# Performance work log

Measured on AMD Instinct MI355X. Metric: run time of the kernel, lower is better.

The kernel has to match this reference:

```python
import jax, jax.numpy as jnp
import numpy as np

B, LQ, LKV = 4, 512, 8192
Q_DIM, KV_DIM = 1024, 512
QK_CH, V_CH, N_HEADS = 256, 256, 8
EPS = 1e-5


def _layernorm(x, g, b):
    m = jnp.mean(x, axis=-1, keepdims=True)
    v = jnp.mean(jnp.square(x - m), axis=-1, keepdims=True)
    return (x - m) * jax.lax.rsqrt(v + EPS) * g + b


def setup_inputs() -> dict:
    key = jax.random.key(0)
    ks = jax.random.split(key, 8)
    hidden_states = jax.random.normal(ks[0], (B, LQ, Q_DIM), dtype=jnp.float32)
    inputs = jax.random.normal(ks[1], (B, LKV, KV_DIM), dtype=jnp.float32)
    # Linear weights stored as [in, out] for x @ W
    Wq = jax.random.normal(ks[2], (Q_DIM, QK_CH), dtype=jnp.float32) * (1.0 / np.sqrt(Q_DIM))
    Wk = jax.random.normal(ks[3], (KV_DIM, QK_CH), dtype=jnp.float32) * (1.0 / np.sqrt(KV_DIM))
    Wv = jax.random.normal(ks[4], (KV_DIM, V_CH), dtype=jnp.float32) * (1.0 / np.sqrt(KV_DIM))
    bq = jnp.zeros((QK_CH,), jnp.float32)
    bk = jax.random.normal(ks[5], (QK_CH,), dtype=jnp.float32) * 0.02
    bv = jax.random.normal(ks[6], (V_CH,), dtype=jnp.float32) * 0.02
    ln1_g = jnp.ones((Q_DIM,), jnp.float32)
    ln1_b = jnp.zeros((Q_DIM,), jnp.float32)
    ln2_g = jnp.ones((KV_DIM,), jnp.float32)
    ln2_b = jnp.zeros((KV_DIM,), jnp.float32)
    return dict(hidden_states=hidden_states, inputs=inputs,
                ln1_g=ln1_g, ln1_b=ln1_b, ln2_g=ln2_g, ln2_b=ln2_b,
                Wq=Wq, bq=bq, Wk=Wk, bk=bk, Wv=Wv, bv=bv)


def reference(hidden_states, inputs, ln1_g, ln1_b, ln2_g, ln2_b,
              Wq, bq, Wk, bk, Wv, bv):
    H = N_HEADS
    dqk = QK_CH // H
    dv = V_CH // H
    hs = _layernorm(hidden_states, ln1_g, ln1_b)          # [B,LQ,Q_DIM]
    inp = _layernorm(inputs, ln2_g, ln2_b)                # [B,LKV,KV_DIM]
    q = (hs @ Wq + bq).reshape(B, LQ, H, dqk)             # [B,LQ,H,dqk]
    k = (inp @ Wk + bk).reshape(B, LKV, H, dqk)           # [B,LKV,H,dqk]
    v = (inp @ Wv + bv).reshape(B, LKV, H, dv)            # [B,LKV,H,dv]
    scores = jnp.einsum('bqhd,bkhd->bhqk', q, k) / np.sqrt(dqk).astype(np.float32)
    probs = jax.nn.softmax(scores, axis=-1)               # [B,H,LQ,LKV] (materialized, as in torch)
    ctx = jnp.einsum('bhqk,bkhd->bqhd', probs, v)         # [B,LQ,H,dv]
    return ctx.reshape(B, LQ, H * dv)
```

## Files before the change

### kernel.cpp

```cpp
#include <hip/hip_runtime.h>
#include <hip/hip_bf16.h>
#include <math.h>

#define NB    4
#define LQ    512
#define LKV   8192
#define QDIM  1024
#define KVDIM 512
#define NH    8
#define EPS_LN 1e-5f
#define SMAX  12.0f

typedef __attribute__((ext_vector_type(8))) short bf16x8;
typedef __attribute__((ext_vector_type(4))) float f32x4;

static __device__ __forceinline__ ushort f2bf(float x) {
    unsigned int u = __builtin_bit_cast(unsigned int, x);
    u += 0x7FFFu + ((u >> 16) & 1u);
    return (ushort)(u >> 16);
}

#if __has_builtin(__builtin_amdgcn_cvt_pk_bf16_f32)
static __device__ __forceinline__ unsigned int pk_bf16(float a, float b) {
    auto r = __builtin_amdgcn_cvt_pk_bf16_f32(a, b);
    return __builtin_bit_cast(unsigned int, r);
}
#else
static __device__ __forceinline__ unsigned int pk_bf16(float a, float b) {
    return (unsigned int)f2bf(a) | ((unsigned int)f2bf(b) << 16);
}
#endif

#if __has_builtin(__builtin_amdgcn_exp2f)
#define EXP2F(x) __builtin_amdgcn_exp2f(x)
#else
#define EXP2F(x) exp2f(x)
#endif

static __device__ __forceinline__ void interleave_swap(unsigned int &x, unsigned int &y, int lane) {
#if __has_builtin(__builtin_amdgcn_permlane32_swap) && __has_builtin(__builtin_amdgcn_permlane16_swap)
    {
        auto r1 = __builtin_amdgcn_permlane32_swap(x, y, false, false);
        auto r2 = __builtin_amdgcn_permlane16_swap(r1[0], r1[1], false, false);
        x = (unsigned int)r2[0];
        y = (unsigned int)r2[1];
    }
#else
    {
        unsigned int xs = (unsigned int)__shfl_xor((int)x, 32, 64);
        unsigned int ys = (unsigned int)__shfl_xor((int)y, 32, 64);
        unsigned int A2 = (lane & 32) ? ys : x;
        unsigned int C2 = (lane & 32) ? y  : xs;
        unsigned int A2x = (unsigned int)__shfl_xor((int)A2, 16, 64);
        unsigned int C2x = (unsigned int)__shfl_xor((int)C2, 16, 64);
        x = (lane & 16) ? C2x : A2;
        y = (lane & 16) ? C2  : A2x;
    }
#endif
}

static __device__ __forceinline__ void gld_lds16(const ushort* g, ushort* l) {
    __builtin_amdgcn_global_load_lds(
        (const __attribute__((address_space(1))) unsigned int*)g,
        (__attribute__((address_space(3))) unsigned int*)l, 16, 0, 0);
}

template<int K>
static __device__ __forceinline__ void ln_norm_row(
    const float* __restrict__ x, const float* __restrict__ g,
    const float* __restrict__ bta, ushort* __restrict__ y, int row, int lane)
{
    const float* xp = x + (size_t)row * K;
    constexpr int NV = K / 256;
    float4 v[NV];
    float s = 0.f;
#pragma unroll
    for (int i = 0; i < NV; ++i) {
        v[i] = *(const float4*)(xp + lane * 4 + i * 256);
        s += v[i].x + v[i].y + v[i].z + v[i].w;
    }
#pragma unroll
    for (int o = 1; o < 64; o <<= 1) s += __shfl_xor(s, o, 64);
    const float mu = s * (1.0f / K);
    float vs = 0.f;
#pragma unroll
    for (int i = 0; i < NV; ++i) {
        float dx = v[i].x - mu, dy = v[i].y - mu, dz = v[i].z - mu, dw = v[i].w - mu;
        vs += dx * dx + dy * dy + dz * dz + dw * dw;
    }
#pragma unroll
    for (int o = 1; o < 64; o <<= 1) vs += __shfl_xor(vs, o, 64);
    const float rs = rsqrtf(vs * (1.0f / K) + EPS_LN);
#pragma unroll
    for (int i = 0; i < NV; ++i) {
        const float4 gv = *(const float4*)(g   + lane * 4 + i * 256);
        const float4 bv = *(const float4*)(bta + lane * 4 + i * 256);
        uint2 o;
        o.x = pk_bf16((v[i].x - mu) * rs * gv.x + bv.x, (v[i].y - mu) * rs * gv.y + bv.y);
        o.y = pk_bf16((v[i].z - mu) * rs * gv.z + bv.z, (v[i].w - mu) * rs * gv.w + bv.w);
        *(uint2*)(y + (size_t)row * K + lane * 4 + i * 256) = o;
    }
}

static __device__ __forceinline__ void ln_stats_row(
    const float* __restrict__ x, float* __restrict__ mean, float* __restrict__ rstd,
    int row, int lane)
{
    const float* xp = x + (size_t)row * QDIM;
    float4 v[4];
    float s = 0.f;
#pragma unroll
    for (int i = 0; i < 4; ++i) {
        v[i] = *(const float4*)(xp + lane * 4 + i * 256);
        s += v[i].x + v[i].y + v[i].z + v[i].w;
    }
#pragma unroll
    for (int o = 1; o < 64; o <<= 1) s += __shfl_xor(s, o, 64);
    const float mu = s * (1.0f / QDIM);
    float vs = 0.f;
#pragma unroll
    for (int i = 0; i < 4; ++i) {
        float dx = v[i].x - mu, dy = v[i].y - mu, dz = v[i].z - mu, dw = v[i].w - mu;
        vs += dx * dx + dy * dy + dz * dz + dw * dw;
    }
#pragma unroll
    for (int o = 1; o < 64; o <<= 1) vs += __shfl_xor(vs, o, 64);
    if (lane == 0) {
        mean[row] = mu;
        rstd[row] = rsqrtf(vs * (1.0f / QDIM) + EPS_LN);
    }
}

static __device__ __forceinline__ void wt_transpose_body(
    const float* __restrict__ src, ushort* __restrict__ dst, int K,
    int kx, int ny, int t, ushort (*Ts)[72])
{
    const int k0 = kx * 64, n0 = ny * 64;
    const int nl = t & 63;
#pragma unroll
    for (int p = 0; p < 16; ++p) {
        const int kl = p * 4 + (t >> 6);
        Ts[nl][kl] = f2bf(src[(size_t)(k0 + kl) * 256 + n0 + nl]);
    }
    __syncthreads();
    const int ck = (t & 7) * 8;
#pragma unroll
    for (int p = 0; p < 2; ++p) {
        const int rn = p * 32 + (t >> 3);
        *(bf16x8*)(dst + (size_t)(n0 + rn) * K + k0 + ck) = *(const bf16x8*)&Ts[rn][ck];
    }
}

__global__ __launch_bounds__(256) void phaseA_kernel(
    const float* __restrict__ inputs, const float* __restrict__ ln2g,
    const float* __restrict__ ln2b,   ushort* __restrict__ Abf,
    const float* __restrict__ hidden, float* __restrict__ mean_h, float* __restrict__ rstd_h,
    const float* __restrict__ Wq, const float* __restrict__ Wk, const float* __restrict__ Wv,
    ushort* __restrict__ WtQ, ushort* __restrict__ WtKV)
{
    __shared__ ushort Ts[64][72];
    const int bid = blockIdx.x;
    const int t = threadIdx.x;
    const int lane = t & 63;
    if (bid < 8192) {
        ln_norm_row<KVDIM>(inputs, ln2g, ln2b, Abf, bid * 4 + (t >> 6), lane);
    } else if (bid < 8704) {
        ln_stats_row(hidden, mean_h, rstd_h, (bid - 8192) * 4 + (t >> 6), lane);
    } else if (bid < 8768) {
        const int p = bid - 8704;
        wt_transpose_body(Wq, WtQ, QDIM, p & 15, p >> 4, t, Ts);
    } else if (bid < 8800) {
        const int p = bid - 8768;
        wt_transpose_body(Wk, WtKV, KVDIM, p & 7, p >> 3, t, Ts);
    } else {
        const int p = bid - 8800;
        wt_transpose_body(Wv, WtKV + (size_t)256 * KVDIM, KVDIM, p & 7, p >> 3, t, Ts);
    }
}

__global__ __launch_bounds__(256, 3) void phaseB_kernel(
    const ushort* __restrict__ Abf, const ushort* __restrict__ WtKV,
    const float* __restrict__ bk, const float* __restrict__ bv,
    ushort* __restrict__ kb, ushort* __restrict__ vt,
    const float* __restrict__ hidden, const float* __restrict__ mean_h,
    const float* __restrict__ rstd_h,
    const float* __restrict__ ln1g, const float* __restrict__ ln1b,
    const ushort* __restrict__ WtQ, const float* __restrict__ bq,
    ushort* __restrict__ qb, float oscale)
{
    __shared__ __align__(16) ushort SMEM[4 * 64 * 72];
    const int bid  = blockIdx.x;
    const int t    = threadIdx.x;
    const int lane = t & 63;
    const int w    = t >> 6;
    const int lq   = lane & 15;
    const int lg   = lane >> 4;
    const int wm   = w >> 1;
    const int wn   = w & 1;

    if (bid < 2048) {
        const int work = ((bid & 7) << 8) | (bid >> 3);
        const int bm = (work >> 2) * 64;
        const int bn = (work & 3) * 128;
        ushort* As = SMEM;
        ushort* Bs = SMEM + 4096;

        const int srow = t >> 3;
        const int scol = ((t & 7) ^ (srow & 7)) * 8;
        const ushort* gA = Abf  + (size_t)(bm + srow) * KVDIM + scol;
        const ushort* gB = WtKV + (size_t)(bn + srow) * KVDIM + scol;

        f32x4 acc[4][2] = {};
        for (int k0 = 0; k0 < KVDIM; k0 += 64) {
            gld_lds16(gA + k0,                      As + t * 8);
            gld_lds16(gA + (size_t)32 * KVDIM + k0, As + 2048 + t * 8);
#pragma unroll
            for (int p = 0; p < 4; ++p)
                gld_lds16(gB + (size_t)(p * 32) * KVDIM + k0, Bs + p * 2048 + t * 8);
            __syncthreads();
#pragma unroll
            for (int kh = 0; kh < 2; ++kh) {
                bf16x8 af[4], bf[2];
#pragma unroll
                for (int mt = 0; mt < 4; ++mt) {
                    const int m = mt * 16 + lq;
                    af[mt] = *(const bf16x8*)(As + m * 64 + (((lg + 4 * kh) ^ (m & 7)) << 3));
                }
#pragma unroll
                for (int nt = 0; nt < 2; ++nt) {
                    const int n = w * 32 + nt * 16 + lq;
                    bf[nt] = *(const bf16x8*)(Bs + n * 64 + (((lg + 4 * kh) ^ (n & 7)) << 3));
                }
#pragma unroll
                for (int mt = 0; mt < 4; ++mt)
#pragma unroll
                    for (int nt = 0; nt < 2; ++nt)
                        acc[mt][nt] = __builtin_amdgcn_mfma_f32_16x16x32_bf16(af[mt], bf[nt], acc[mt][nt], 0, 0, 0);
            }
            __syncthreads();
        }
        const int bidx = bm >> 13;
        const int tokb = bm & 8191;
        const int nc0  = bn + w * 32;

        if (bn < 256) {
            ushort* Cs = SMEM + w * 2560;
#pragma unroll
            for (int nt = 0; nt < 2; ++nt) {
                const int n_l = nt * 16 + lq;
                const float bias = bk[nc0 + n_l];
#pragma unroll
                for (int mt = 0; mt < 4; ++mt)
#pragma unroll
                    for (int r = 0; r < 4; ++r)
                        Cs[(mt * 16 + lg * 4 + r) * 40 + n_l] = f2bf(acc[mt][nt][r] + bias);
            }
            const int r0 = lane >> 2;
            const int ck = (lane & 3) * 8;
            const int h  = nc0 >> 5;
            const size_t obase = (((size_t)(bidx * NH + h) << 13) + tokb) * 32 + ck;
#pragma unroll
            for (int p = 0; p < 4; ++p) {
                const int row = p * 16 + r0;
                *(bf16x8*)(kb + obase + (size_t)row * 32) = *(const bf16x8*)&Cs[row * 40 + ck];
            }
        } else {
            ushort* Cs = SMEM + w * 2560;
#pragma unroll
            for (int nt = 0; nt < 2; ++nt) {
                const int n_l = nt * 16 + lq;
                const float bias = bv[(nc0 - 256) + n_l];
#pragma unroll
                for (int mt = 0; mt < 4; ++mt) {
                    uint2 o;
                    o.x = pk_bf16(acc[mt][nt][0] + bias, acc[mt][nt][1] + bias);
                    o.y = pk_bf16(acc[mt][nt][2] + bias, acc[mt][nt][3] + bias);
                    *(uint2*)&Cs[n_l * 72 + mt * 16 + lg * 4] = o;
                }
            }
            const int r0 = lane >> 3;
            const int cm = (lane & 7) * 8;
            const int nv0 = nc0 - 256;
            const int h  = nv0 >> 5;
            const int tokc = tokb + cm;
#pragma unroll
            for (int p = 0; p < 4; ++p) {
                const int row = p * 8 + r0;
                *(bf16x8*)(vt + ((size_t)(bidx * NH + h) * 32 + row) * LKV + tokc) =
                    *(const bf16x8*)&Cs[row * 72 + cm];
            }
        }
    } else {
        const int p  = bid - 2048;
        const int bm = (p >> 2) * 64;
        const int bn = (p & 3) * 64;
        ushort* As = SMEM;
        ushort* Bs = SMEM + 4096;

        const int srow = t >> 3;
        const int scol = ((t & 7) ^ (srow & 7)) * 8;
        const ushort* gB = WtQ + (size_t)(bn + srow) * QDIM + scol;
        ushort* lB  = Bs + t * 8;
        ushort* lA0 = As + t * 8;
        ushort* lA1 = As + 2048 + t * 8;

        const int r0 = bm + srow;
        const float mu0 = mean_h[r0],      rs0 = rstd_h[r0];
        const float mu1 = mean_h[r0 + 32], rs1 = rstd_h[r0 + 32];
        const float* xA0 = hidden + (size_t)r0 * QDIM + scol;
        const float* xA1 = xA0 + (size_t)32 * QDIM;

        f32x4 acc[2][2] = {};
        for (int k0 = 0; k0 < QDIM; k0 += 64) {
            gld_lds16(gB + k0,                      lB);
            gld_lds16(gB + (size_t)32 * QDIM + k0,  lB + 2048);
            const float4 a0 = *(const float4*)(xA0 + k0);
            const float4 a1 = *(const float4*)(xA0 + k0 + 4);
            const float4 c0 = *(const float4*)(xA1 + k0);
            const float4 c1 = *(const float4*)(xA1 + k0 + 4);
            const float4 g0 = *(const float4*)(ln1g + k0 + scol);
            const float4 g1 = *(const float4*)(ln1g + k0 + scol + 4);
            const float4 d0 = *(const float4*)(ln1b + k0 + scol);
            const float4 d1 = *(const float4*)(ln1b + k0 + scol + 4);
            uint4 w0, w1;
            w0.x = pk_bf16((a0.x - mu0) * rs0 * g0.x + d0.x, (a0.y - mu0) * rs0 * g0.y + d0.y);
            w0.y = pk_bf16((a0.z - mu0) * rs0 * g0.z + d0.z, (a0.w - mu0) * rs0 * g0.w + d0.w);
            w0.z = pk_bf16((a1.x - mu0) * rs0 * g1.x + d1.x, (a1.y - mu0) * rs0 * g1.y + d1.y);
            w0.w = pk_bf16((a1.z - mu0) * rs0 * g1.z + d1.z, (a1.w - mu0) * rs0 * g1.w + d1.w);
            w1.x = pk_bf16((c0.x - mu1) * rs1 * g0.x + d0.x, (c0.y - mu1) * rs1 * g0.y + d0.y);
            w1.y = pk_bf16((c0.z - mu1) * rs1 * g0.z + d0.z, (c0.w - mu1) * rs1 * g0.w + d0.w);
            w1.z = pk_bf16((c1.x - mu1) * rs1 * g1.x + d1.x, (c1.y - mu1) * rs1 * g1.y + d1.y);
            w1.w = pk_bf16((c1.z - mu1) * rs1 * g1.z + d1.z, (c1.w - mu1) * rs1 * g1.w + d1.w);
            *(uint4*)lA0 = w0;
            *(uint4*)lA1 = w1;
            __syncthreads();
#pragma unroll
            for (int kh = 0; kh < 2; ++kh) {
                bf16x8 af[2], bf[2];
#pragma unroll
                for (int mt = 0; mt < 2; ++mt) {
                    const int m = wm * 32 + mt * 16 + lq;
                    af[mt] = *(const bf16x8*)(As + m * 64 + (((lg + 4 * kh) ^ (m & 7)) << 3));
                }
#pragma unroll
                for (int nt = 0; nt < 2; ++nt) {
                    const int n = wn * 32 + nt * 16 + lq;
                    bf[nt] = *(const bf16x8*)(Bs + n * 64 + (((lg + 4 * kh) ^ (n & 7)) << 3));
                }
#pragma unroll
                for (int mt = 0; mt < 2; ++mt)
#pragma unroll
                    for (int nt = 0; nt < 2; ++nt)
                        acc[mt][nt] = __builtin_amdgcn_mfma_f32_16x16x32_bf16(af[mt], bf[nt], acc[mt][nt], 0, 0, 0);
            }
            __syncthreads();
        }

#pragma unroll
        for (int nt = 0; nt < 2; ++nt) {
            const int n = bn + wn * 32 + nt * 16 + lq;
            const int h = n >> 5, d = n & 31;
            const float bias = bq[n];
#pragma unroll
            for (int mt = 0; mt < 2; ++mt) {
                const int m0   = bm + wm * 32 + mt * 16 + lg * 4;
                const int bidx = m0 >> 9;
                const int tok  = m0 & 511;
                const size_t base = (((size_t)(bidx * NH + h) << 9) + tok) * 32 + d;
#pragma unroll
                for (int r = 0; r < 4; ++r)
                    qb[base + (size_t)r * 32] = f2bf((acc[mt][nt][r] + bias) * oscale);
            }
        }
    }
}

#define NQ 4
__global__ __launch_bounds__(256, 3) void attn_mfma_kernel(
    const ushort* __restrict__ Qb,
    const ushort* __restrict__ Kb,
    const ushort* __restrict__ Vt,
    float* __restrict__ Opart,
    float* __restrict__ lpart)
{
    const int bid = blockIdx.x;
    const int xcd = bid & 7;
    const int u   = bid >> 3;
    const int bhw = u >> 5;
    const int r2  = u & 31;
    const int qt  = r2 >> 2;
    const int quarter = r2 & 3;
    const int bh  = (bhw << 3) | xcd;
    const int t = threadIdx.x, w = t >> 6, lane = t & 63;
    const int lq = lane & 15, lg = lane >> 4;

    __shared__ __align__(16) float Ob[2 * 64 * 36];
    __shared__ float lbuf[4][64];

    bf16x8 qfrag[NQ];
    const size_t qbase = ((size_t)bh * LQ + qt * 64) * 32;
#pragma unroll
    for (int n = 0; n < NQ; ++n)
        qfrag[n] = *(const bf16x8*)(Qb + qbase + (size_t)(n * 16 + lq) * 32 + lg * 8);

    const int kv0 = quarter * 2048 + w * 512;
    const ushort* KpA = Kb + ((size_t)bh * LKV + kv0 + lq) * 32 + lg * 8;
    const ushort* VpA = Vt + ((size_t)bh * 32 + lq) * LKV + kv0 + lg * 8;

    f32x4 oacc[2][NQ] = {};
    float l_part[NQ] = {};
    const f32x4 cM = {-SMAX, -SMAX, -SMAX, -SMAX};

    for (int kt = 0; kt < 512; kt += 64) {
        bf16x8 kc[4];
#pragma unroll
        for (int m = 0; m < 4; ++m)
            kc[m] = *(const bf16x8*)(KpA + (size_t)(kt + m * 16) * 32);
        bf16x8 vc[2][2];
#pragma unroll
        for (int dt = 0; dt < 2; ++dt)
#pragma unroll
            for (int z = 0; z < 2; ++z)
                vc[dt][z] = *(const bf16x8*)(VpA + (size_t)(dt * 16) * LKV + kt + z * 32);

#pragma unroll
        for (int z = 0; z < 2; ++z) {
            f32x4 s2[2][NQ];
#pragma unroll
            for (int mm = 0; mm < 2; ++mm)
#pragma unroll
                for (int n = 0; n < NQ; ++n)
                    s2[mm][n] = __builtin_amdgcn_mfma_f32_16x16x32_bf16(kc[2 * z + mm], qfrag[n], cM, 0, 0, 0);

            bf16x8 pfz[NQ];
#pragma unroll
            for (int n = 0; n < NQ; ++n) {
                const float e0 = EXP2F(s2[0][n][0]);
                const float e1 = EXP2F(s2[0][n][1]);
                const float e2 = EXP2F(s2[0][n][2]);
                const float e3 = EXP2F(s2[0][n][3]);
                const float f0 = EXP2F(s2[1][n][0]);
                const float f1 = EXP2F(s2[1][n][1]);
                const float f2 = EXP2F(s2[1][n][2]);
                const float f3 = EXP2F(s2[1][n][3]);
                l_part[n] += ((e0 + e1) + (e2 + e3)) + ((f0 + f1) + (f2 + f3));
                unsigned int wa = pk_bf16(e0, e1);
                unsigned int wb = pk_bf16(e2, e3);
                unsigned int wc = pk_bf16(f0, f1);
                unsigned int wd = pk_bf16(f2, f3);
                interleave_swap(wa, wc, lane);
                interleave_swap(wb, wd, lane);
                uint4 wv;
                wv.x = wa; wv.y = wb; wv.z = wc; wv.w = wd;
                pfz[n] = __builtin_bit_cast(bf16x8, wv);
            }

#pragma unroll
            for (int dt = 0; dt < 2; ++dt)
#pragma unroll
                for (int n = 0; n < NQ; ++n)
                    oacc[dt][n] = __builtin_amdgcn_mfma_f32_16x16x32_bf16(vc[dt][z], pfz[n], oacc[dt][n], 0, 0, 0);
        }
    }

#pragma unroll
    for (int n = 0; n < NQ; ++n) {
        l_part[n] += __shfl_xor(l_part[n], 16);
        l_part[n] += __shfl_xor(l_part[n], 32);
    }
    if (lg == 0) {
#pragma unroll
        for (int n = 0; n < NQ; ++n)
            lbuf[w][n * 16 + lq] = l_part[n];
    }
    if (w >= 2) {
#pragma unroll
        for (int n = 0; n < NQ; ++n)
#pragma unroll
            for (int dt = 0; dt < 2; ++dt)
                *(f32x4*)&Ob[((size_t)(w - 2) * 64 + n * 16 + lq) * 36 + dt * 16 + lg * 4] = oacc[dt][n];
    }
    __syncthreads();
    if (w < 2) {
#pragma unroll
        for (int n = 0; n < NQ; ++n)
#pragma unroll
            for (int dt = 0; dt < 2; ++dt) {
                float* p = &Ob[((size_t)w * 64 + n * 16 + lq) * 36 + dt * 16 + lg * 4];
                f32x4 v = *(f32x4*)p;
                v += oacc[dt][n];
                *(f32x4*)p = v;
            }
    }
    __syncthreads();
    {
        const int pidx = (quarter * 32 + bh) * 8 + qt;
        const int q  = t >> 3;
        const int d0 = (t & 7) * 4;
#pragma unroll
        for (int rh = 0; rh < 2; ++rh) {
            const int row = q + rh * 32;
            f32x4 s0 = *(const f32x4*)&Ob[((size_t)row) * 36 + d0];
            f32x4 s1 = *(const f32x4*)&Ob[((size_t)(64 + row)) * 36 + d0];
            s0 += s1;
            *(f32x4*)(Opart + (size_t)pidx * 2048 + row * 32 + d0) = s0;
            if ((t & 7) == 0) {
                float gl = lbuf[0][row] + lbuf[1][row] + lbuf[2][row] + lbuf[3][row];
                lpart[(size_t)pidx * 64 + row] = gl;
            }
        }
    }
}

__global__ __launch_bounds__(256) void attn_combine_kernel(
    const float* __restrict__ Opart, const float* __restrict__ lpart,
    float* __restrict__ Out)
{
    const int cb = blockIdx.x;
    const int bh = cb >> 3, qt = cb & 7;
    const int b = bh >> 3, h = bh & 7;
    const int t = threadIdx.x;
    const int q = t >> 3;
    const int dq = (t & 7) * 4;
#pragma unroll
    for (int rh = 0; rh < 2; ++rh) {
        const int row = q + rh * 32;
        float4 o = {0.f, 0.f, 0.f, 0.f};
        float l = 0.f;
#pragma unroll
        for (int j = 0; j < 4; ++j) {
            const size_t pidx = (size_t)((j * 32 + bh) * 8 + qt);
            const float4 a = *(const float4*)(Opart + pidx * 2048 + row * 32 + dq);
            o.x += a.x; o.y += a.y; o.z += a.z; o.w += a.w;
            l += lpart[pidx * 64 + row];
        }
        const float inv = 1.0f / l;
        o.x *= inv; o.y *= inv; o.z *= inv; o.w *= inv;
        *(float4*)(Out + ((size_t)b * LQ + qt * 64 + row) * 256 + h * 32 + dq) = o;
    }
}

extern "C" void kernel_launch(void* const* d_in, const int* in_sizes, int n_in,
                              void* d_out, int out_size, void* d_ws, size_t ws_size,
                              hipStream_t stream)
{
    const float* hidden = (const float*)d_in[0];
    const float* inputs = (const float*)d_in[1];
    const float* ln1g   = (const float*)d_in[2];
    const float* ln1b   = (const float*)d_in[3];
    const float* ln2g   = (const float*)d_in[4];
    const float* ln2b   = (const float*)d_in[5];
    const float* Wq     = (const float*)d_in[6];
    const float* bq     = (const float*)d_in[7];
    const float* Wk     = (const float*)d_in[8];
    const float* bk     = (const float*)d_in[9];
    const float* Wv     = (const float*)d_in[10];
    const float* bv     = (const float*)d_in[11];
    float* out = (float*)d_out;

    char* wsb = (char*)d_ws;
    ushort* qb     = (ushort*)(wsb);
    ushort* WtKV   = (ushort*)(wsb + (1u << 20));
    ushort* WtQ    = (ushort*)(wsb + (1u << 20) + (512u << 10));
    float*  mean_h = (float*)(wsb + (2u << 20));
    float*  rstd_h = (float*)(wsb + (2u << 20) + 8192);
    ushort* kb     = (ushort*)(wsb + (2u << 20) + 16384);
    ushort* vt     = (ushort*)(wsb + (18u << 20) + 16384);
    ushort* Abf    = (ushort*)(wsb + (34u << 20) + 16384);

    float* Opart = (float*)Abf;
    float* lpart = Opart + (size_t)4 * 32 * 8 * 2048;

    const float oscale = 0.2550540226496112f;

    phaseA_kernel<<<8832, 256, 0, stream>>>(inputs, ln2g, ln2b, Abf,
                                            hidden, mean_h, rstd_h,
                                            Wq, Wk, Wv, WtQ, WtKV);
    phaseB_kernel<<<2176, 256, 0, stream>>>(Abf, WtKV, bk, bv, kb, vt,
                                            hidden, mean_h, rstd_h, ln1g, ln1b,
                                            WtQ, bq, qb, oscale);
    attn_mfma_kernel<<<1024, 256, 0, stream>>>(qb, kb, vt, Opart, lpart);
    attn_combine_kernel<<<256, 256, 0, stream>>>(Opart, lpart, out);
}
```

Measured before the change: 205.6 us.

## Double query tile per attention block and interleave QK/PV MFMAs per query group

Each attention block now handles 128 query rows (NQ=8) instead of 64, halving the grid and the number of times each K/V tile is loaded from memory. The QK MFMA, exp and PV MFMA are now fused per query fragment instead of running as separate batched phases, which shortens live ranges for score registers. In exchange, register pressure rises (launch bounds drop to 2 blocks per CU), there are fewer blocks to fill the device, and the combine kernel and partial buffers are resized to match.

```diff
diff --git a/kernel.cpp b/kernel.cpp
--- a/kernel.cpp
+++ b/kernel.cpp
@@ -375,8 +375,8 @@
     }
 }
 
-#define NQ 4
-__global__ __launch_bounds__(256, 3) void attn_mfma_kernel(
+#define NQ 8
+__global__ __launch_bounds__(256, 2) void attn_mfma_kernel(
     const ushort* __restrict__ Qb,
     const ushort* __restrict__ Kb,
     const ushort* __restrict__ Vt,
@@ -386,19 +386,19 @@
     const int bid = blockIdx.x;
     const int xcd = bid & 7;
     const int u   = bid >> 3;
-    const int bhw = u >> 5;
-    const int r2  = u & 31;
+    const int bhw = u >> 4;
+    const int r2  = u & 15;
     const int qt  = r2 >> 2;
     const int quarter = r2 & 3;
     const int bh  = (bhw << 3) | xcd;
     const int t = threadIdx.x, w = t >> 6, lane = t & 63;
     const int lq = lane & 15, lg = lane >> 4;
 
-    __shared__ __align__(16) float Ob[2 * 64 * 36];
-    __shared__ float lbuf[4][64];
+    __shared__ __align__(16) float Ob[2 * 128 * 36];
+    __shared__ float lbuf[4][128];
 
     bf16x8 qfrag[NQ];
-    const size_t qbase = ((size_t)bh * LQ + qt * 64) * 32;
+    const size_t qbase = ((size_t)bh * LQ + qt * 128) * 32;
 #pragma unroll
     for (int n = 0; n < NQ; ++n)
         qfrag[n] = *(const bf16x8*)(Qb + qbase + (size_t)(n * 16 + lq) * 32 + lg * 8);
@@ -425,24 +425,18 @@
 
 #pragma unroll
         for (int z = 0; z < 2; ++z) {
-            f32x4 s2[2][NQ];
-#pragma unroll
-            for (int mm = 0; mm < 2; ++mm)
-#pragma unroll
-                for (int n = 0; n < NQ; ++n)
-                    s2[mm][n] = __builtin_amdgcn_mfma_f32_16x16x32_bf16(kc[2 * z + mm], qfrag[n], cM, 0, 0, 0);
-
-            bf16x8 pfz[NQ];
 #pragma unroll
             for (int n = 0; n < NQ; ++n) {
-                const float e0 = EXP2F(s2[0][n][0]);
-                const float e1 = EXP2F(s2[0][n][1]);
-                const float e2 = EXP2F(s2[0][n][2]);
-                const float e3 = EXP2F(s2[0][n][3]);
-                const float f0 = EXP2F(s2[1][n][0]);
-                const float f1 = EXP2F(s2[1][n][1]);
-                const float f2 = EXP2F(s2[1][n][2]);
-                const float f3 = EXP2F(s2[1][n][3]);
+                f32x4 s0 = __builtin_amdgcn_mfma_f32_16x16x32_bf16(kc[2 * z],     qfrag[n], cM, 0, 0, 0);
+                f32x4 s1 = __builtin_amdgcn_mfma_f32_16x16x32_bf16(kc[2 * z + 1], qfrag[n], cM, 0, 0, 0);
+                const float e0 = EXP2F(s0[0]);
+                const float e1 = EXP2F(s0[1]);
+                const float e2 = EXP2F(s0[2]);
+                const float e3 = EXP2F(s0[3]);
+                const float f0 = EXP2F(s1[0]);
+                const float f1 = EXP2F(s1[1]);
+                const float f2 = EXP2F(s1[2]);
+                const float f3 = EXP2F(s1[3]);
                 l_part[n] += ((e0 + e1) + (e2 + e3)) + ((f0 + f1) + (f2 + f3));
                 unsigned int wa = pk_bf16(e0, e1);
                 unsigned int wb = pk_bf16(e2, e3);
@@ -452,14 +446,10 @@
                 interleave_swap(wb, wd, lane);
                 uint4 wv;
                 wv.x = wa; wv.y = wb; wv.z = wc; wv.w = wd;
-                pfz[n] = __builtin_bit_cast(bf16x8, wv);
-            }
-
-#pragma unroll
-            for (int dt = 0; dt < 2; ++dt)
-#pragma unroll
-                for (int n = 0; n < NQ; ++n)
-                    oacc[dt][n] = __builtin_amdgcn_mfma_f32_16x16x32_bf16(vc[dt][z], pfz[n], oacc[dt][n], 0, 0, 0);
+                const bf16x8 pfz = __builtin_bit_cast(bf16x8, wv);
+                oacc[0][n] = __builtin_amdgcn_mfma_f32_16x16x32_bf16(vc[0][z], pfz, oacc[0][n], 0, 0, 0);
+                oacc[1][n] = __builtin_amdgcn_mfma_f32_16x16x32_bf16(vc[1][z], pfz, oacc[1][n], 0, 0, 0);
+            }
         }
     }
 
@@ -478,7 +468,7 @@
         for (int n = 0; n < NQ; ++n)
 #pragma unroll
             for (int dt = 0; dt < 2; ++dt)
-                *(f32x4*)&Ob[((size_t)(w - 2) * 64 + n * 16 + lq) * 36 + dt * 16 + lg * 4] = oacc[dt][n];
+                *(f32x4*)&Ob[((size_t)(w - 2) * 128 + n * 16 + lq) * 36 + dt * 16 + lg * 4] = oacc[dt][n];
     }
     __syncthreads();
     if (w < 2) {
@@ -486,7 +476,7 @@
         for (int n = 0; n < NQ; ++n)
 #pragma unroll
             for (int dt = 0; dt < 2; ++dt) {
-                float* p = &Ob[((size_t)w * 64 + n * 16 + lq) * 36 + dt * 16 + lg * 4];
+                float* p = &Ob[((size_t)w * 128 + n * 16 + lq) * 36 + dt * 16 + lg * 4];
                 f32x4 v = *(f32x4*)p;
                 v += oacc[dt][n];
                 *(f32x4*)p = v;
@@ -494,19 +484,19 @@
     }
     __syncthreads();
     {
-        const int pidx = (quarter * 32 + bh) * 8 + qt;
+        const int pidx = (quarter * 32 + bh) * 4 + qt;
         const int q  = t >> 3;
         const int d0 = (t & 7) * 4;
 #pragma unroll
-        for (int rh = 0; rh < 2; ++rh) {
+        for (int rh = 0; rh < 4; ++rh) {
             const int row = q + rh * 32;
             f32x4 s0 = *(const f32x4*)&Ob[((size_t)row) * 36 + d0];
-            f32x4 s1 = *(const f32x4*)&Ob[((size_t)(64 + row)) * 36 + d0];
+            f32x4 s1 = *(const f32x4*)&Ob[((size_t)(128 + row)) * 36 + d0];
             s0 += s1;
-            *(f32x4*)(Opart + (size_t)pidx * 2048 + row * 32 + d0) = s0;
+            *(f32x4*)(Opart + (size_t)pidx * 4096 + row * 32 + d0) = s0;
             if ((t & 7) == 0) {
                 float gl = lbuf[0][row] + lbuf[1][row] + lbuf[2][row] + lbuf[3][row];
-                lpart[(size_t)pidx * 64 + row] = gl;
+                lpart[(size_t)pidx * 128 + row] = gl;
             }
         }
     }
@@ -517,26 +507,26 @@
     float* __restrict__ Out)
 {
     const int cb = blockIdx.x;
-    const int bh = cb >> 3, qt = cb & 7;
+    const int bh = cb >> 2, qt = cb & 3;
     const int b = bh >> 3, h = bh & 7;
     const int t = threadIdx.x;
     const int q = t >> 3;
     const int dq = (t & 7) * 4;
 #pragma unroll
-    for (int rh = 0; rh < 2; ++rh) {
+    for (int rh = 0; rh < 4; ++rh) {
         const int row = q + rh * 32;
         float4 o = {0.f, 0.f, 0.f, 0.f};
         float l = 0.f;
 #pragma unroll
         for (int j = 0; j < 4; ++j) {
-            const size_t pidx = (size_t)((j * 32 + bh) * 8 + qt);
-            const float4 a = *(const float4*)(Opart + pidx * 2048 + row * 32 + dq);
+            const size_t pidx = (size_t)((j * 32 + bh) * 4 + qt);
+            const float4 a = *(const float4*)(Opart + pidx * 4096 + row * 32 + dq);
             o.x += a.x; o.y += a.y; o.z += a.z; o.w += a.w;
-            l += lpart[pidx * 64 + row];
+            l += lpart[pidx * 128 + row];
         }
         const float inv = 1.0f / l;
         o.x *= inv; o.y *= inv; o.z *= inv; o.w *= inv;
-        *(float4*)(Out + ((size_t)b * LQ + qt * 64 + row) * 256 + h * 32 + dq) = o;
+        *(float4*)(Out + ((size_t)b * LQ + qt * 128 + row) * 256 + h * 32 + dq) = o;
     }
 }
 
@@ -569,7 +559,7 @@
     ushort* Abf    = (ushort*)(wsb + (34u << 20) + 16384);
 
     float* Opart = (float*)Abf;
-    float* lpart = Opart + (size_t)4 * 32 * 8 * 2048;
+    float* lpart = Opart + (size_t)4 * 32 * 4 * 4096;
 
     const float oscale = 0.2550540226496112f;
 
@@ -579,6 +569,6 @@
     phaseB_kernel<<<2176, 256, 0, stream>>>(Abf, WtKV, bk, bv, kb, vt,
                                             hidden, mean_h, rstd_h, ln1g, ln1b,
                                             WtQ, bq, qb, oscale);
-    attn_mfma_kernel<<<1024, 256, 0, stream>>>(qb, kb, vt, Opart, lpart);
-    attn_combine_kernel<<<256, 256, 0, stream>>>(Opart, lpart, out);
-}
+    attn_mfma_kernel<<<512, 256, 0, stream>>>(qb, kb, vt, Opart, lpart);
+    attn_combine_kernel<<<128, 256, 0, stream>>>(Opart, lpart, out);
+}
```

After: 202.0 us. Within noise of the previous version (-1.8%).
